# Kernel optimization log

Measured on AMD Instinct MI355X. Metric: run time of the kernel, lower is better.

The kernel has to match this reference:

```python
import jax, jax.numpy as jnp
import numpy as np

N = 100000  # number of nodes
SELF_LOOP_W = 2.0  # improved=True in PyG GCNConv


def gcn_conv(x, edge_index, W, b):
    # x: [N, Fin], edge_index: [2, E] (row=src, col=dst), W: [Fin, Fout], b: [Fout]
    src, dst = edge_index[0], edge_index[1]
    h = x @ W  # [N, Fout]
    # degree with improved self-loops (weight 2.0)
    ones = jnp.ones(src.shape, dtype=h.dtype)
    deg = jax.ops.segment_sum(ones, dst, num_segments=N) + SELF_LOOP_W
    dinv = jnp.where(deg > 0, jax.lax.rsqrt(deg), 0.0)
    norm = dinv[src] * dinv[dst]  # [E]
    agg = jax.ops.segment_sum(h[src] * norm[:, None], dst, num_segments=N)
    # self-loop contribution: weight 2.0, norm = dinv_i * 2 * dinv_i
    agg = agg + h * (SELF_LOOP_W * dinv * dinv)[:, None]
    return agg + b


def setup_inputs() -> dict:
    key = jax.random.key(0)
    ks = jax.random.split(key, 6)
    x = jax.random.normal(ks[0], (N, 64), dtype=jnp.float32)
    edge_index = jax.random.randint(ks[1], (2, 1600000), 0, N, dtype=jnp.int64)
    W1 = jax.random.normal(ks[2], (64, 64), dtype=jnp.float32) * 0.1
    b1 = jax.random.normal(ks[3], (64,), dtype=jnp.float32) * 0.1
    W2 = jax.random.normal(ks[4], (64, 32), dtype=jnp.float32) * 0.1
    b2 = jax.random.normal(ks[5], (32,), dtype=jnp.float32) * 0.1
    return {"x": x, "edge_index": edge_index, "W1": W1, "b1": b1, "W2": W2, "b2": b2}


def reference(x, edge_index, W1, b1, W2, b2):
    h1 = jax.nn.relu(gcn_conv(x, edge_index, W1, b1))
    feature_map = h1
    out = gcn_conv(h1, edge_index, W2, b2)
    return (out, feature_map)
```

## Files before the change

### kernel.cpp

```cpp
#include <hip/hip_runtime.h>

#define N_NODES 100000
#define E_EDGES 1600000

#define BSHIFT 7
#define BSIZE 128
#define NBUCK ((N_NODES + BSIZE - 1) / BSIZE)
#define STAGE_TPB 512
#define STAGE_EPT 8
#define STAGE_CHUNK (STAGE_TPB * STAGE_EPT)
#define NREP 2
#define BUCKET_CAP 4096

typedef __attribute__((ext_vector_type(8))) short short8;
typedef __attribute__((ext_vector_type(4))) float float4v;

__device__ inline unsigned short f2bf(float f) {
    union { float f; unsigned u; } t; t.f = f;
    unsigned r = (t.u + 0x7fffu + ((t.u >> 16) & 1u)) >> 16;
    return (unsigned short)r;
}
__device__ inline float bf2f(unsigned short h) {
    union { unsigned u; float f; } t; t.u = ((unsigned)h) << 16; return t.f;
}
__device__ inline unsigned pack_bf16x2(float a, float b) {
    return (unsigned)f2bf(a) | ((unsigned)f2bf(b) << 16);
}
__device__ inline float bf_lo(unsigned u) { union { unsigned u; float f; } t; t.u = u << 16; return t.f; }
__device__ inline float bf_hi(unsigned u) { union { unsigned u; float f; } t; t.u = u & 0xffff0000u; return t.f; }

__global__ void __launch_bounds__(STAGE_TPB) stage_kernel(
    const int* __restrict__ src, const int* __restrict__ dst,
    int* __restrict__ gcursor, unsigned* __restrict__ staged, int E) {
    __shared__ int hist[NREP][NBUCK];
    __shared__ int base[NREP][NBUCK];
    const int tid = threadIdx.x;
    const int rep = (tid >> 8) & (NREP - 1);
    const int e0 = blockIdx.x * STAGE_CHUNK;
    for (int i = tid; i < NREP * NBUCK; i += STAGE_TPB) ((int*)hist)[i] = 0;
    __syncthreads();
    int d[STAGE_EPT], s[STAGE_EPT];
#pragma unroll
    for (int k = 0; k < STAGE_EPT; ++k) {
        int e = e0 + k * STAGE_TPB + tid;
        if (e < E) {
            d[k] = dst[e];
            s[k] = src[e];
            atomicAdd(&hist[rep][d[k] >> BSHIFT], 1);
        } else {
            d[k] = -1;
        }
    }
    __syncthreads();
    for (int i = tid; i < NBUCK; i += STAGE_TPB) {
        int h0 = hist[0][i], h1 = hist[1][i];
        int t = h0 + h1;
        if (t > 0) {
            int g = atomicAdd(&gcursor[i], t);
            int abs0 = i * BUCKET_CAP + g;
            base[0][i] = abs0;
            base[1][i] = abs0 + h0;
        }
    }
    __syncthreads();
#pragma unroll
    for (int k = 0; k < STAGE_EPT; ++k) {
        if (d[k] >= 0) {
            int b = d[k] >> BSHIFT;
            int pos = atomicAdd(&base[rep][b], 1);
            if (pos < (b + 1) * BUCKET_CAP)
                staged[pos] = (unsigned)s[k] | ((unsigned)(d[k] & (BSIZE - 1)) << 17);
        }
    }
}

__global__ void bscan_kernel(const int* __restrict__ gcursor, int* __restrict__ boff) {
    __shared__ int s[1024];
    const int tid = threadIdx.x;
    int v = 0;
    if (tid < NBUCK) {
        v = gcursor[tid];
        if (v > BUCKET_CAP) v = BUCKET_CAP;
    }
    s[tid] = v;
    __syncthreads();
    for (int off = 1; off < 1024; off <<= 1) {
        int t = (tid >= off) ? s[tid - off] : 0;
        __syncthreads();
        s[tid] += t;
        __syncthreads();
    }
    if (tid < NBUCK) boff[tid] = s[tid] - v;
    if (tid == NBUCK - 1) boff[NBUCK] = s[tid];
}

__global__ void bucket_csr_kernel(const unsigned* __restrict__ staged,
                                  const int* __restrict__ boff,
                                  int2* __restrict__ nodeinfo, float* __restrict__ dinv,
                                  int* __restrict__ csrc, int n) {
    __shared__ int ldeg[BSIZE];
    __shared__ int lrp[BSIZE];
    __shared__ int lcnt[BSIZE];
    __shared__ unsigned lrec[BUCKET_CAP];
    __shared__ int lsrc[BUCKET_CAP];
    const int b = blockIdx.x;
    const int node0 = b * BSIZE;
    const int nn = min(BSIZE, n - node0);
    const int tid = threadIdx.x;
    if (tid < BSIZE) { ldeg[tid] = 0; lcnt[tid] = 0; }
    __syncthreads();
    const int ebase = boff[b];
    const int ecnt = min(boff[b + 1] - ebase, BUCKET_CAP);
    const int sbase = b * BUCKET_CAP;
    for (int i = tid; i < ecnt; i += 256) {
        unsigned r = staged[sbase + i];
        lrec[i] = r;
        atomicAdd(&ldeg[r >> 17], 1);
    }
    __syncthreads();
    int mydeg = (tid < BSIZE) ? ldeg[tid] : 0;
    if (tid < BSIZE) lrp[tid] = mydeg;
    __syncthreads();
    for (int off = 1; off < BSIZE; off <<= 1) {
        int v = 0;
        if (tid < BSIZE && tid >= off) v = lrp[tid - off];
        __syncthreads();
        if (tid < BSIZE) lrp[tid] += v;
        __syncthreads();
    }
    if (tid < BSIZE) {
        int ex = lrp[tid] - mydeg;
        lrp[tid] = ex;
        if (tid < nn) {
            nodeinfo[node0 + tid] = make_int2(ebase + ex, mydeg);
            dinv[node0 + tid] = rsqrtf((float)mydeg + 2.0f);
        }
    }
    __syncthreads();
    for (int i = tid; i < ecnt; i += 256) {
        unsigned r = lrec[i];
        int dl = (int)(r >> 17);
        int sv = (int)(r & 0x1FFFFu);
        int pos = lrp[dl] + atomicAdd(&lcnt[dl], 1);
        if (pos < BUCKET_CAP) lsrc[pos] = sv;
    }
    __syncthreads();
    for (int i = tid; i < ecnt; i += 256)
        csrc[ebase + i] = lsrc[i];
}

template <int FOUT>
__global__ void __launch_bounds__(256) linear_mfma_kernel(
    const float* __restrict__ X, const float* __restrict__ W,
    const float* __restrict__ dinv, unsigned* __restrict__ HS, int n) {
    constexpr int NT = FOUT / 16;
    const int NTILES_M = n / 16;
    const int lane = threadIdx.x & 63;
    const int gwave = blockIdx.x * 4 + (threadIdx.x >> 6);
    const int nwaves = gridDim.x * 4;
    const int m = lane & 15;
    const int q = lane >> 4;

    short8 Bhi[2][NT], Blo[2][NT];
#pragma unroll
    for (int ks = 0; ks < 2; ++ks)
#pragma unroll
        for (int nt = 0; nt < NT; ++nt) {
            short8 bh, bl;
#pragma unroll
            for (int j = 0; j < 8; ++j) {
                int k = ks * 32 + q * 8 + j;
                float wv = W[k * FOUT + nt * 16 + m];
                unsigned short h = f2bf(wv);
                bh[j] = (short)h;
                bl[j] = (short)f2bf(wv - bf2f(h));
            }
            Bhi[ks][nt] = bh;
            Blo[ks][nt] = bl;
        }

    for (int tile = gwave; tile < NTILES_M; tile += nwaves) {
        const int row0 = tile * 16;
        float4v C[NT];
#pragma unroll
        for (int nt = 0; nt < NT; ++nt) C[nt] = (float4v){0.f, 0.f, 0.f, 0.f};
#pragma unroll
        for (int ks = 0; ks < 2; ++ks) {
            const float* xp = X + (size_t)(row0 + m) * 64 + ks * 32 + q * 8;
            float4v x0 = *(const float4v*)xp;
            float4v x1 = *(const float4v*)(xp + 4);
            short8 Ahi, Alo;
#pragma unroll
            for (int j = 0; j < 4; ++j) {
                unsigned short h0 = f2bf(x0[j]);
                Ahi[j] = (short)h0;
                Alo[j] = (short)f2bf(x0[j] - bf2f(h0));
                unsigned short h1 = f2bf(x1[j]);
                Ahi[4 + j] = (short)h1;
                Alo[4 + j] = (short)f2bf(x1[j] - bf2f(h1));
            }
#pragma unroll
            for (int nt = 0; nt < NT; ++nt) {
                C[nt] = __builtin_amdgcn_mfma_f32_16x16x32_bf16(Ahi, Bhi[ks][nt], C[nt], 0, 0, 0);
                C[nt] = __builtin_amdgcn_mfma_f32_16x16x32_bf16(Alo, Bhi[ks][nt], C[nt], 0, 0, 0);
                C[nt] = __builtin_amdgcn_mfma_f32_16x16x32_bf16(Ahi, Blo[ks][nt], C[nt], 0, 0, 0);
            }
        }
        if constexpr (FOUT == 64) {
#pragma unroll
            for (int t = 0; t < 2; ++t) {
#pragma unroll
                for (int reg = 0; reg < 4; ++reg) {
                    int r = row0 + q * 4 + reg;
                    float di = dinv[r];
                    unsigned u = pack_bf16x2(C[t][reg] * di, C[t + 2][reg] * di);
                    HS[(size_t)r * 32 + t * 16 + m] = u;
                }
            }
        } else {
#pragma unroll
            for (int reg = 0; reg < 4; ++reg) {
                int r = row0 + q * 4 + reg;
                float di = dinv[r];
                unsigned u = pack_bf16x2(C[0][reg] * di, C[1][reg] * di);
                HS[(size_t)r * 16 + m] = u;
            }
        }
    }
}

template <int G, bool RELU>
__global__ void gather_kernel(const int2* __restrict__ nodeinfo,
                              const int* __restrict__ csrc, const unsigned* __restrict__ HS,
                              const float* __restrict__ dinv, const float* __restrict__ bias,
                              float* __restrict__ OUT, int n) {
    constexpr int NPB = 256 / G;
    int node = blockIdx.x * NPB + (threadIdx.x / G);
    int l = threadIdx.x % G;
    if (node >= n) return;
    int2 ni = nodeinfo[node];
    int start = ni.x, cnt = ni.y;
    unsigned us = HS[(size_t)node * G + l];
    float a0 = 2.0f * bf_lo(us);
    float a1 = 2.0f * bf_hi(us);
    float b0 = 0.0f, b1 = 0.0f;
    int j = start, end = start + cnt;
    for (; j + 7 < end; j += 8) {
        int s0 = csrc[j],     s1 = csrc[j + 1], s2 = csrc[j + 2], s3 = csrc[j + 3];
        int s4 = csrc[j + 4], s5 = csrc[j + 5], s6 = csrc[j + 6], s7 = csrc[j + 7];
        unsigned u0 = HS[(size_t)s0 * G + l];
        unsigned u1 = HS[(size_t)s1 * G + l];
        unsigned u2 = HS[(size_t)s2 * G + l];
        unsigned u3 = HS[(size_t)s3 * G + l];
        unsigned u4 = HS[(size_t)s4 * G + l];
        unsigned u5 = HS[(size_t)s5 * G + l];
        unsigned u6 = HS[(size_t)s6 * G + l];
        unsigned u7 = HS[(size_t)s7 * G + l];
        a0 += bf_lo(u0) + bf_lo(u1) + bf_lo(u2) + bf_lo(u3);
        a1 += bf_hi(u0) + bf_hi(u1) + bf_hi(u2) + bf_hi(u3);
        b0 += bf_lo(u4) + bf_lo(u5) + bf_lo(u6) + bf_lo(u7);
        b1 += bf_hi(u4) + bf_hi(u5) + bf_hi(u6) + bf_hi(u7);
    }
    for (; j + 3 < end; j += 4) {
        int s0 = csrc[j], s1 = csrc[j + 1], s2 = csrc[j + 2], s3 = csrc[j + 3];
        unsigned u0 = HS[(size_t)s0 * G + l];
        unsigned u1 = HS[(size_t)s1 * G + l];
        unsigned u2 = HS[(size_t)s2 * G + l];
        unsigned u3 = HS[(size_t)s3 * G + l];
        a0 += bf_lo(u0) + bf_lo(u1);
        a1 += bf_hi(u0) + bf_hi(u1);
        b0 += bf_lo(u2) + bf_lo(u3);
        b1 += bf_hi(u2) + bf_hi(u3);
    }
    for (; j < end; ++j) {
        unsigned u = HS[(size_t)csrc[j] * G + l];
        a0 += bf_lo(u);
        a1 += bf_hi(u);
    }
    a0 += b0;
    a1 += b1;
    float dd = dinv[node];
    float o0 = a0 * dd + bias[l];
    float o1 = a1 * dd + bias[G + l];
    if (RELU) { o0 = fmaxf(o0, 0.0f); o1 = fmaxf(o1, 0.0f); }
    OUT[(size_t)node * (2 * G) + l] = o0;
    OUT[(size_t)node * (2 * G) + G + l] = o1;
}

extern "C" void kernel_launch(void* const* d_in, const int* in_sizes, int n_in,
                              void* d_out, int out_size, void* d_ws, size_t ws_size,
                              hipStream_t stream) {
    const float* x  = (const float*)d_in[0];
    const int*   ei = (const int*)d_in[1];
    const float* W1 = (const float*)d_in[2];
    const float* b1 = (const float*)d_in[3];
    const float* W2 = (const float*)d_in[4];
    const float* b2 = (const float*)d_in[5];

    const int* srcp = ei;
    const int* dstp = ei + E_EDGES;

    float* out = (float*)d_out;
    float* fm  = (float*)d_out + N_NODES * 32;

    char* w = (char*)d_ws;
    int*      gcursor  = (int*)w;       w += sizeof(int) * NBUCK;
    int*      boff     = (int*)w;       w += sizeof(int) * (NBUCK + 1);
    int2*     nodeinfo = (int2*)w;      w += sizeof(int2) * N_NODES;
    float*    dinv     = (float*)w;     w += sizeof(float) * N_NODES;
    int*      csrc     = (int*)w;       w += sizeof(int) * E_EDGES;
    unsigned* staged   = (unsigned*)w;  w += sizeof(unsigned) * (size_t)NBUCK * BUCKET_CAP;
    unsigned* HS1      = (unsigned*)w;  w += sizeof(unsigned) * (size_t)N_NODES * 32;
    unsigned* HS2      = (unsigned*)w;  w += sizeof(unsigned) * (size_t)N_NODES * 16;

    hipMemsetAsync(gcursor, 0, sizeof(int) * NBUCK, stream);
    stage_kernel<<<(E_EDGES + STAGE_CHUNK - 1) / STAGE_CHUNK, STAGE_TPB, 0, stream>>>(
        srcp, dstp, gcursor, staged, E_EDGES);
    bscan_kernel<<<1, 1024, 0, stream>>>(gcursor, boff);
    bucket_csr_kernel<<<NBUCK, 256, 0, stream>>>(staged, boff, nodeinfo, dinv, csrc, N_NODES);

    linear_mfma_kernel<64><<<512, 256, 0, stream>>>(x, W1, dinv, HS1, N_NODES);
    gather_kernel<32, true><<<(N_NODES + 7) / 8, 256, 0, stream>>>(
        nodeinfo, csrc, HS1, dinv, b1, fm, N_NODES);

    linear_mfma_kernel<32><<<512, 256, 0, stream>>>(fm, W2, dinv, HS2, N_NODES);
    gather_kernel<16, false><<<(N_NODES + 15) / 16, 256, 0, stream>>>(
        nodeinfo, csrc, HS2, dinv, b2, out, N_NODES);
}
```

Measured before the change: 220.4 us.

## Split gather feature tables into column chunks for smaller random-access working set

Stores the scaled hidden features as two separate column-chunk planes (each 64 bytes per node) instead of one interleaved row, and launches gather blocks that each handle one chunk over 64 nodes. Block indices interleave chunks so both halves of a node tile are processed close together. The intent is to shrink the per-pass random-access footprint and the bytes fetched per gathered neighbour, so that more of each table stays in cache. The cost is that every node's CSR neighbour list is now read twice, once per chunk, and the second layer reads 16-bit values, which gives narrower loads.

```diff
diff --git a/kernel.cpp b/kernel.cpp
--- a/kernel.cpp
+++ b/kernel.cpp
@@ -149,11 +149,10 @@
         csrc[ebase + i] = lsrc[i];
 }
 
-template <int FOUT>
-__global__ void __launch_bounds__(256) linear_mfma_kernel(
+__global__ void __launch_bounds__(256) linear_mfma64_kernel(
     const float* __restrict__ X, const float* __restrict__ W,
     const float* __restrict__ dinv, unsigned* __restrict__ HS, int n) {
-    constexpr int NT = FOUT / 16;
+    constexpr int NT = 4;
     const int NTILES_M = n / 16;
     const int lane = threadIdx.x & 63;
     const int gwave = blockIdx.x * 4 + (threadIdx.x >> 6);
@@ -170,7 +169,7 @@
 #pragma unroll
             for (int j = 0; j < 8; ++j) {
                 int k = ks * 32 + q * 8 + j;
-                float wv = W[k * FOUT + nt * 16 + m];
+                float wv = W[k * 64 + nt * 16 + m];
                 unsigned short h = f2bf(wv);
                 bh[j] = (short)h;
                 bl[j] = (short)f2bf(wv - bf2f(h));
@@ -206,38 +205,100 @@
                 C[nt] = __builtin_amdgcn_mfma_f32_16x16x32_bf16(Ahi, Blo[ks][nt], C[nt], 0, 0, 0);
             }
         }
-        if constexpr (FOUT == 64) {
-#pragma unroll
-            for (int t = 0; t < 2; ++t) {
-#pragma unroll
-                for (int reg = 0; reg < 4; ++reg) {
-                    int r = row0 + q * 4 + reg;
-                    float di = dinv[r];
-                    unsigned u = pack_bf16x2(C[t][reg] * di, C[t + 2][reg] * di);
-                    HS[(size_t)r * 32 + t * 16 + m] = u;
-                }
-            }
-        } else {
+#pragma unroll
+        for (int ch = 0; ch < 2; ++ch) {
 #pragma unroll
             for (int reg = 0; reg < 4; ++reg) {
                 int r = row0 + q * 4 + reg;
                 float di = dinv[r];
-                unsigned u = pack_bf16x2(C[0][reg] * di, C[1][reg] * di);
-                HS[(size_t)r * 16 + m] = u;
-            }
-        }
-    }
-}
-
-template <int G, bool RELU>
-__global__ void gather_kernel(const int2* __restrict__ nodeinfo,
-                              const int* __restrict__ csrc, const unsigned* __restrict__ HS,
-                              const float* __restrict__ dinv, const float* __restrict__ bias,
-                              float* __restrict__ OUT, int n) {
-    constexpr int NPB = 256 / G;
-    int node = blockIdx.x * NPB + (threadIdx.x / G);
+                unsigned u = pack_bf16x2(C[2 * ch][reg] * di, C[2 * ch + 1][reg] * di);
+                HS[(size_t)ch * n * 16 + (size_t)r * 16 + m] = u;
+            }
+        }
+    }
+}
+
+__global__ void __launch_bounds__(256) linear_mfma32_kernel(
+    const float* __restrict__ X, const float* __restrict__ W,
+    const float* __restrict__ dinv, unsigned short* __restrict__ HS, int n) {
+    constexpr int NT = 2;
+    const int NTILES_M = n / 16;
+    const int lane = threadIdx.x & 63;
+    const int gwave = blockIdx.x * 4 + (threadIdx.x >> 6);
+    const int nwaves = gridDim.x * 4;
+    const int m = lane & 15;
+    const int q = lane >> 4;
+
+    short8 Bhi[2][NT], Blo[2][NT];
+#pragma unroll
+    for (int ks = 0; ks < 2; ++ks)
+#pragma unroll
+        for (int nt = 0; nt < NT; ++nt) {
+            short8 bh, bl;
+#pragma unroll
+            for (int j = 0; j < 8; ++j) {
+                int k = ks * 32 + q * 8 + j;
+                float wv = W[k * 32 + nt * 16 + m];
+                unsigned short h = f2bf(wv);
+                bh[j] = (short)h;
+                bl[j] = (short)f2bf(wv - bf2f(h));
+            }
+            Bhi[ks][nt] = bh;
+            Blo[ks][nt] = bl;
+        }
+
+    for (int tile = gwave; tile < NTILES_M; tile += nwaves) {
+        const int row0 = tile * 16;
+        float4v C[NT];
+#pragma unroll
+        for (int nt = 0; nt < NT; ++nt) C[nt] = (float4v){0.f, 0.f, 0.f, 0.f};
+#pragma unroll
+        for (int ks = 0; ks < 2; ++ks) {
+            const float* xp = X + (size_t)(row0 + m) * 64 + ks * 32 + q * 8;
+            float4v x0 = *(const float4v*)xp;
+            float4v x1 = *(const float4v*)(xp + 4);
+            short8 Ahi, Alo;
+#pragma unroll
+            for (int j = 0; j < 4; ++j) {
+                unsigned short h0 = f2bf(x0[j]);
+                Ahi[j] = (short)h0;
+                Alo[j] = (short)f2bf(x0[j] - bf2f(h0));
+                unsigned short h1 = f2bf(x1[j]);
+                Ahi[4 + j] = (short)h1;
+                Alo[4 + j] = (short)f2bf(x1[j] - bf2f(h1));
+            }
+#pragma unroll
+            for (int nt = 0; nt < NT; ++nt) {
+                C[nt] = __builtin_amdgcn_mfma_f32_16x16x32_bf16(Ahi, Bhi[ks][nt], C[nt], 0, 0, 0);
+                C[nt] = __builtin_amdgcn_mfma_f32_16x16x32_bf16(Alo, Bhi[ks][nt], C[nt], 0, 0, 0);
+                C[nt] = __builtin_amdgcn_mfma_f32_16x16x32_bf16(Ahi, Blo[ks][nt], C[nt], 0, 0, 0);
+            }
+        }
+#pragma unroll
+        for (int c = 0; c < 2; ++c) {
+#pragma unroll
+            for (int reg = 0; reg < 4; ++reg) {
+                int r = row0 + q * 4 + reg;
+                float di = dinv[r];
+                HS[(size_t)c * n * 16 + (size_t)r * 16 + m] = f2bf(C[c][reg] * di);
+            }
+        }
+    }
+}
+
+__global__ void gather1_kernel(const int2* __restrict__ nodeinfo,
+                               const int* __restrict__ csrc, const unsigned* __restrict__ HS0,
+                               const float* __restrict__ dinv, const float* __restrict__ bias,
+                               float* __restrict__ OUT, int n) {
+    constexpr int G = 16;
+    const int r = blockIdx.x & 7;
+    const int chunk = r >> 2;
+    const int tile = (blockIdx.x >> 3) * 4 + (r & 3);
+    int node = tile * 16 + (threadIdx.x / G);
     int l = threadIdx.x % G;
     if (node >= n) return;
+    const unsigned* __restrict__ HS = HS0 + (size_t)chunk * n * G;
+    const float* __restrict__ bias0 = bias + 32 * chunk;
     int2 ni = nodeinfo[node];
     int start = ni.x, cnt = ni.y;
     unsigned us = HS[(size_t)node * G + l];
@@ -280,11 +341,55 @@
     a0 += b0;
     a1 += b1;
     float dd = dinv[node];
-    float o0 = a0 * dd + bias[l];
-    float o1 = a1 * dd + bias[G + l];
-    if (RELU) { o0 = fmaxf(o0, 0.0f); o1 = fmaxf(o1, 0.0f); }
-    OUT[(size_t)node * (2 * G) + l] = o0;
-    OUT[(size_t)node * (2 * G) + G + l] = o1;
+    float o0 = a0 * dd + bias0[l];
+    float o1 = a1 * dd + bias0[16 + l];
+    o0 = fmaxf(o0, 0.0f);
+    o1 = fmaxf(o1, 0.0f);
+    OUT[(size_t)node * 64 + 32 * chunk + l] = o0;
+    OUT[(size_t)node * 64 + 32 * chunk + 16 + l] = o1;
+}
+
+__global__ void gather2_kernel(const int2* __restrict__ nodeinfo,
+                               const int* __restrict__ csrc, const unsigned short* __restrict__ HS0,
+                               const float* __restrict__ dinv, const float* __restrict__ bias,
+                               float* __restrict__ OUT, int n) {
+    constexpr int G = 16;
+    const int r = blockIdx.x & 7;
+    const int chunk = r >> 2;
+    const int tile = (blockIdx.x >> 3) * 4 + (r & 3);
+    int node = tile * 16 + (threadIdx.x / G);
+    int l = threadIdx.x % G;
+    if (node >= n) return;
+    const unsigned short* __restrict__ HS = HS0 + (size_t)chunk * n * G;
+    int2 ni = nodeinfo[node];
+    int start = ni.x, cnt = ni.y;
+    float a0 = 2.0f * bf2f(HS[(size_t)node * G + l]);
+    float b0 = 0.0f;
+    int j = start, end = start + cnt;
+    for (; j + 7 < end; j += 8) {
+        int s0 = csrc[j],     s1 = csrc[j + 1], s2 = csrc[j + 2], s3 = csrc[j + 3];
+        int s4 = csrc[j + 4], s5 = csrc[j + 5], s6 = csrc[j + 6], s7 = csrc[j + 7];
+        float v0 = bf2f(HS[(size_t)s0 * G + l]);
+        float v1 = bf2f(HS[(size_t)s1 * G + l]);
+        float v2 = bf2f(HS[(size_t)s2 * G + l]);
+        float v3 = bf2f(HS[(size_t)s3 * G + l]);
+        float v4 = bf2f(HS[(size_t)s4 * G + l]);
+        float v5 = bf2f(HS[(size_t)s5 * G + l]);
+        float v6 = bf2f(HS[(size_t)s6 * G + l]);
+        float v7 = bf2f(HS[(size_t)s7 * G + l]);
+        a0 += v0 + v1 + v2 + v3;
+        b0 += v4 + v5 + v6 + v7;
+    }
+    for (; j + 3 < end; j += 4) {
+        int s0 = csrc[j], s1 = csrc[j + 1], s2 = csrc[j + 2], s3 = csrc[j + 3];
+        a0 += bf2f(HS[(size_t)s0 * G + l]) + bf2f(HS[(size_t)s1 * G + l]);
+        b0 += bf2f(HS[(size_t)s2 * G + l]) + bf2f(HS[(size_t)s3 * G + l]);
+    }
+    for (; j < end; ++j)
+        a0 += bf2f(HS[(size_t)csrc[j] * G + l]);
+    a0 += b0;
+    float o0 = a0 * dinv[node] + bias[16 * chunk + l];
+    OUT[(size_t)node * 32 + 16 * chunk + l] = o0;
 }
 
 extern "C" void kernel_launch(void* const* d_in, const int* in_sizes, int n_in,
@@ -304,14 +409,16 @@
     float* fm  = (float*)d_out + N_NODES * 32;
 
     char* w = (char*)d_ws;
-    int*      gcursor  = (int*)w;       w += sizeof(int) * NBUCK;
-    int*      boff     = (int*)w;       w += sizeof(int) * (NBUCK + 1);
-    int2*     nodeinfo = (int2*)w;      w += sizeof(int2) * N_NODES;
-    float*    dinv     = (float*)w;     w += sizeof(float) * N_NODES;
-    int*      csrc     = (int*)w;       w += sizeof(int) * E_EDGES;
-    unsigned* staged   = (unsigned*)w;  w += sizeof(unsigned) * (size_t)NBUCK * BUCKET_CAP;
-    unsigned* HS1      = (unsigned*)w;  w += sizeof(unsigned) * (size_t)N_NODES * 32;
-    unsigned* HS2      = (unsigned*)w;  w += sizeof(unsigned) * (size_t)N_NODES * 16;
+    int*            gcursor  = (int*)w;            w += sizeof(int) * NBUCK;
+    int*            boff     = (int*)w;            w += sizeof(int) * (NBUCK + 1);
+    int2*           nodeinfo = (int2*)w;           w += sizeof(int2) * N_NODES;
+    float*          dinv     = (float*)w;          w += sizeof(float) * N_NODES;
+    int*            csrc     = (int*)w;            w += sizeof(int) * E_EDGES;
+    unsigned*       staged   = (unsigned*)w;       w += sizeof(unsigned) * (size_t)NBUCK * BUCKET_CAP;
+    unsigned*       HS1      = (unsigned*)w;       w += sizeof(unsigned) * (size_t)N_NODES * 32;
+    unsigned short* HS2      = (unsigned short*)w; w += sizeof(unsigned short) * (size_t)N_NODES * 32;
+
+    const int NGATHER = ((N_NODES / 16 + 3) / 4) * 8;
 
     hipMemsetAsync(gcursor, 0, sizeof(int) * NBUCK, stream);
     stage_kernel<<<(E_EDGES + STAGE_CHUNK - 1) / STAGE_CHUNK, STAGE_TPB, 0, stream>>>(
@@ -319,11 +426,9 @@
     bscan_kernel<<<1, 1024, 0, stream>>>(gcursor, boff);
     bucket_csr_kernel<<<NBUCK, 256, 0, stream>>>(staged, boff, nodeinfo, dinv, csrc, N_NODES);
 
-    linear_mfma_kernel<64><<<512, 256, 0, stream>>>(x, W1, dinv, HS1, N_NODES);
-    gather_kernel<32, true><<<(N_NODES + 7) / 8, 256, 0, stream>>>(
-        nodeinfo, csrc, HS1, dinv, b1, fm, N_NODES);
-
-    linear_mfma_kernel<32><<<512, 256, 0, stream>>>(fm, W2, dinv, HS2, N_NODES);
-    gather_kernel<16, false><<<(N_NODES + 15) / 16, 256, 0, stream>>>(
-        nodeinfo, csrc, HS2, dinv, b2, out, N_NODES);
-}
+    linear_mfma64_kernel<<<512, 256, 0, stream>>>(x, W1, dinv, HS1, N_NODES);
+    gather1_kernel<<<NGATHER, 256, 0, stream>>>(nodeinfo, csrc, HS1, dinv, b1, fm, N_NODES);
+
+    linear_mfma32_kernel<<<512, 256, 0, stream>>>(fm, W2, dinv, HS2, N_NODES);
+    gather2_kernel<<<NGATHER, 256, 0, stream>>>(nodeinfo, csrc, HS2, dinv, b2, out, N_NODES);
+}
```

Result: slower. 228.7 us (+3.7%).
